# Performance work log

Hardware: AMD Instinct MI355X
Metric: run time of the kernel (lower is better)

Reference implementation:

```python
import jax, jax.numpy as jnp
import numpy as np
import math

B, N, CS, CZ, H, HD, PQ, PV = 1, 512, 1024, 128, 12, 16, 4, 8
INF, EPS = 1e5, 1e-8


def _quat_to_rot(q):
    q = q / jnp.linalg.norm(q, axis=-1, keepdims=True)
    w, x, y, z = q[..., 0], q[..., 1], q[..., 2], q[..., 3]
    R = jnp.stack([
        1 - 2 * (y * y + z * z), 2 * (x * y - w * z), 2 * (x * z + w * y),
        2 * (x * y + w * z), 1 - 2 * (x * x + z * z), 2 * (y * z - w * x),
        2 * (x * z - w * y), 2 * (y * z + w * x), 1 - 2 * (x * x + y * y)
    ], axis=-1)
    return R.reshape(q.shape[:-1] + (3, 3))


def _split3(x):
    # torch.split into 3 chunks along last dim, then stack on new last dim
    d = x.shape[-1] // 3
    return jnp.stack((x[..., :d], x[..., d:2 * d], x[..., 2 * d:]), axis=-1)


def setup_inputs():
    key = jax.random.key(0)
    ks = jax.random.split(key, 12)

    def lin(k, din, dout):
        kw, kb = jax.random.split(k)
        W = jax.random.normal(kw, (din, dout), jnp.float32) / np.float32(np.sqrt(din))
        b = jax.random.normal(kb, (dout,), jnp.float32) * 0.01
        return W, b

    s = jax.random.normal(ks[0], (B, N, CS), jnp.float32)
    z = jax.random.normal(ks[1], (B, N, N, CZ), jnp.float32)
    rot = _quat_to_rot(jax.random.normal(ks[2], (B, N, 4), jnp.float32))
    trans = jax.random.normal(ks[3], (B, N, 3), jnp.float32) * 10.0
    mask = jnp.ones((B, N), jnp.float32)

    Wq, bq = lin(ks[4], CS, H * HD)
    Wkv, bkv = lin(ks[5], CS, 2 * H * HD)
    Wqp, bqp = lin(ks[6], CS, H * PQ * 3)
    Wkvp, bkvp = lin(ks[7], CS, H * (PQ + PV) * 3)
    Wb, bb = lin(ks[8], CZ, H)
    head_w = jax.random.normal(ks[9], (H,), jnp.float32) * 0.5
    Wout, bout = lin(ks[10], H * (CZ + HD + PV * 4), CS)

    return dict(s=s, z=z, rot=rot, trans=trans, mask=mask,
                Wq=Wq, bq=bq, Wkv=Wkv, bkv=bkv, Wqp=Wqp, bqp=bqp,
                Wkvp=Wkvp, bkvp=bkvp, Wb=Wb, bb=bb, head_w=head_w,
                Wout=Wout, bout=bout)


def _ipa(s, z, rot, trans, mask, Wq, bq, Wkv, bkv, Wqp, bqp, Wkvp, bkvp, Wb, bb, head_w, Wout, bout):
    # scalar q, k, v : [B, N, H, HD]
    q = (s @ Wq + bq).reshape(B, N, H, HD)
    kv = (s @ Wkv + bkv).reshape(B, N, H, 2 * HD)
    k, v = kv[..., :HD], kv[..., HD:]

    # point q/k/v in global frame: p' = R p + t
    q_pts = _split3(s @ Wqp + bqp)                      # [B, N, H*PQ, 3]
    q_pts = jnp.einsum('bnij,bnpj->bnpi', rot, q_pts) + trans[:, :, None, :]
    q_pts = q_pts.reshape(B, N, H, PQ, 3)

    kv_pts = _split3(s @ Wkvp + bkvp)                   # [B, N, H*(PQ+PV), 3]
    kv_pts = jnp.einsum('bnij,bnpj->bnpi', rot, kv_pts) + trans[:, :, None, :]
    kv_pts = kv_pts.reshape(B, N, H, PQ + PV, 3)
    k_pts, v_pts = kv_pts[..., :PQ, :], kv_pts[..., PQ:, :]

    # pair bias [B, N, N, H]
    b = z @ Wb + bb

    # scalar attention logits [B, H, N, N]
    a = jnp.einsum('bihd,bjhd->bhij', q, k) * np.float32(math.sqrt(1.0 / (3 * HD)))
    a = a + np.float32(math.sqrt(1.0 / 3)) * jnp.transpose(b, (0, 3, 1, 2))

    # point-distance attention: [B, N, N, H, PQ]
    diff = q_pts[:, :, None] - k_pts[:, None]           # [B, N, N, H, PQ, 3]
    pt_att = jnp.sum(diff * diff, axis=-1)
    hw = jax.nn.softplus(head_w) * np.float32(math.sqrt(1.0 / (3 * (PQ * 9.0 / 2))))
    pt_att = jnp.sum(pt_att * hw[:, None], axis=-1) * (-0.5)   # [B, N, N, H]
    a = a + jnp.transpose(pt_att, (0, 3, 1, 2))

    square_mask = INF * (mask[:, :, None] * mask[:, None, :] - 1.0)  # [B, N, N]
    a = jax.nn.softmax(a + square_mask[:, None], axis=-1)            # [B, H, N, N]

    # scalar output [B, N, H*HD]
    o = jnp.einsum('bhij,bjhd->bihd', a, v).reshape(B, N, H * HD)

    # point output, back to local frame: R^T (p - t)
    o_pt = jnp.einsum('bhij,bjhpc->bihpc', a, v_pts)                 # [B, N, H, PV, 3]
    o_pt = jnp.einsum('bnji,bnhpj->bnhpi', rot, o_pt - trans[:, :, None, None, :])
    o_pt_norm = jnp.sqrt(jnp.sum(o_pt * o_pt, axis=-1) + EPS).reshape(B, N, H * PV)
    o_pt_r = o_pt.reshape(B, N, H * PV, 3)

    # pair output [B, N, H*CZ]
    o_pair = jnp.einsum('bhij,bijc->bihc', a, z).reshape(B, N, H * CZ)

    cat = jnp.concatenate(
        (o, o_pt_r[..., 0], o_pt_r[..., 1], o_pt_r[..., 2], o_pt_norm, o_pair), axis=-1)
    return cat @ Wout + bout


def reference(s, z, rot, trans, mask, Wq, bq, Wkv, bkv, Wqp, bqp, Wkvp, bkvp, Wb, bb, head_w, Wout, bout):
    return _ipa(s, z, rot, trans, mask, Wq, bq, Wkv, bkv, Wqp, bqp, Wkvp, bkvp, Wb, bb, head_w, Wout, bout)
```

## Files before the change

### kernel.cpp

```cpp
#include <hip/hip_runtime.h>
#include <hip/hip_bf16.h>

#define N 512
#define CS 1024
#define CZ 128
#define H 12
#define HD 16
#define KC 2112

__device__ int sniff_f32(const unsigned short* p) {
    int bad = 0;
    for (int i = 0; i < 32; ++i) {
        unsigned short u = p[i];
        int e = (u >> 7) & 0xFF;
        if (e == 0xFF || e >= 141 || (e <= 27 && (u & 0x7FFFu) != 0)) bad++;
    }
    return bad > 0;
}

__device__ __forceinline__ float ld(const void* p, int i, int f32) {
    return f32 ? ((const float*)p)[i]
               : __bfloat162float(((const __hip_bfloat16*)p)[i]);
}

__device__ __forceinline__ float bfu(unsigned short u) {
    return __bfloat162float(*(const __hip_bfloat16*)&u);
}

typedef __attribute__((ext_vector_type(8))) short bf16x8;
typedef __attribute__((ext_vector_type(4))) float f32x4;
typedef __attribute__((ext_vector_type(8))) unsigned short u16x8;

__device__ __forceinline__ unsigned int split_bf16(float x) {
    __hip_bfloat16 hb = __float2bfloat16(x);
    float hf = __bfloat162float(hb);
    __hip_bfloat16 lb = __float2bfloat16(x - hf);
    unsigned int h = *reinterpret_cast<unsigned short*>(&hb);
    unsigned int l = *reinterpret_cast<unsigned short*>(&lb);
    return h | (l << 16);
}

__device__ __forceinline__ void wcat_resolve(int col,
        const void* Wq, const void* Wkv, const void* Wqp, const void* Wkvp,
        const void*& W, int& cc, int& ldim) {
    if (col < 192)      { W = Wq;   cc = col;       ldim = 192; }
    else if (col < 576) { W = Wkv;  cc = col - 192; ldim = 384; }
    else if (col < 720) { W = Wqp;  cc = col - 576; ldim = 144; }
    else                { W = Wkvp; cc = col - 720; ldim = 432; }
}

__global__ void prep_w(const void* Wq, const void* Wkv, const void* Wqp,
                       const void* Wkvp, const void* Wout, const void* s,
                       unsigned short* WcTh, unsigned short* WcTl,
                       unsigned short* WoTh, unsigned short* WoTl)
{
    __shared__ unsigned short th[32][33], tl[32][33];
    __shared__ int flag;
    int t = threadIdx.x;
    if (t == 0) flag = sniff_f32((const unsigned short*)s);
    __syncthreads();
    int f32 = flag;
    int tx = t & 31, ty = t >> 5;
    int b = blockIdx.x;
    if (b < 1152) {
        int ct = b % 36, kt = b / 36;
        int c0 = ct * 32, k0 = kt * 32;
        #pragma unroll
        for (int r = 0; r < 4; ++r) {
            int k = k0 + ty + 8 * r, c = c0 + tx;
            const void* W; int cc, ldim;
            wcat_resolve(c, Wq, Wkv, Wqp, Wkvp, W, cc, ldim);
            unsigned int pe = split_bf16(ld(W, k * ldim + cc, f32));
            th[ty + 8 * r][tx] = (unsigned short)pe;
            tl[ty + 8 * r][tx] = (unsigned short)(pe >> 16);
        }
        __syncthreads();
        #pragma unroll
        for (int r = 0; r < 4; ++r) {
            int c = c0 + ty + 8 * r, k = k0 + tx;
            WcTh[c * CS + k] = th[tx][ty + 8 * r];
            WcTl[c * CS + k] = tl[tx][ty + 8 * r];
        }
    } else {
        int bb = b - 1152;
        int ct = bb & 31, kt = bb >> 5;
        int c0 = ct * 32, k0 = kt * 32;
        #pragma unroll
        for (int r = 0; r < 4; ++r) {
            int k = k0 + ty + 8 * r, c = c0 + tx;
            unsigned int pe = split_bf16(ld(Wout, k * CS + c, f32));
            th[ty + 8 * r][tx] = (unsigned short)pe;
            tl[ty + 8 * r][tx] = (unsigned short)(pe >> 16);
        }
        __syncthreads();
        #pragma unroll
        for (int r = 0; r < 4; ++r) {
            int c = c0 + ty + 8 * r, k = k0 + tx;
            WoTh[c * KC + k] = th[tx][ty + 8 * r];
            WoTl[c * KC + k] = tl[tx][ty + 8 * r];
        }
    }
}

__global__ void proj_gemm(const void* s, const unsigned short* BTh,
                          const unsigned short* BTl, float* rawP)
{
    __shared__ int flag;
    int t = threadIdx.x;
    int bn = blockIdx.x;
    int bm = blockIdx.y;
    if (t == 0) flag = sniff_f32((const unsigned short*)s);
    __syncthreads();
    int f32 = flag;

    int w  = t >> 6, l = t & 63;
    int wm = w >> 1, wn = w & 1;
    int lr = l & 15, lq = l >> 4;

    int arow = bm * 32 + wm * 16 + lr;
    int bcol = bn * 64 + wn * 32 + lr;
    const unsigned short* bh = BTh + bcol * CS;
    const unsigned short* bl = BTl + bcol * CS;

    f32x4 acc0 = {0.f, 0.f, 0.f, 0.f};
    f32x4 acc1 = {0.f, 0.f, 0.f, 0.f};

    #pragma unroll 2
    for (int kt = 0; kt < CS / 32; ++kt) {
        int kk = kt * 32 + lq * 8;
        u16x8 ah, al;
        if (f32) {
            const float* ap = (const float*)s + arow * CS + kk;
            #pragma unroll
            for (int e = 0; e < 8; ++e) {
                unsigned int pe = split_bf16(ap[e]);
                ah[e] = (unsigned short)pe; al[e] = (unsigned short)(pe >> 16);
            }
        } else {
            ah = *(const u16x8*)((const unsigned short*)s + arow * CS + kk);
            #pragma unroll
            for (int e = 0; e < 8; ++e) al[e] = 0;
        }
        bf16x8 b0h = *(const bf16x8*)(bh + kk);
        bf16x8 b0l = *(const bf16x8*)(bl + kk);
        bf16x8 b1h = *(const bf16x8*)(bh + 16 * CS + kk);
        bf16x8 b1l = *(const bf16x8*)(bl + 16 * CS + kk);
        bf16x8 a_h = *(bf16x8*)&ah;
        bf16x8 a_l = *(bf16x8*)&al;
        acc0 = __builtin_amdgcn_mfma_f32_16x16x32_bf16(a_h, b0h, acc0, 0, 0, 0);
        acc0 = __builtin_amdgcn_mfma_f32_16x16x32_bf16(a_h, b0l, acc0, 0, 0, 0);
        acc0 = __builtin_amdgcn_mfma_f32_16x16x32_bf16(a_l, b0h, acc0, 0, 0, 0);
        acc1 = __builtin_amdgcn_mfma_f32_16x16x32_bf16(a_h, b1h, acc1, 0, 0, 0);
        acc1 = __builtin_amdgcn_mfma_f32_16x16x32_bf16(a_h, b1l, acc1, 0, 0, 0);
        acc1 = __builtin_amdgcn_mfma_f32_16x16x32_bf16(a_l, b1h, acc1, 0, 0, 0);
    }

    int col0 = bn * 64 + wn * 32 + lr;
    int row0 = bm * 32 + wm * 16 + lq * 4;
    #pragma unroll
    for (int r = 0; r < 4; ++r) {
        rawP[(row0 + r) * 1152 + col0]      = acc0[r];
        rawP[(row0 + r) * 1152 + col0 + 16] = acc1[r];
    }
}

__global__ void proj_post(const float* rawP,
                          const void* bq, const void* bkv,
                          const void* bqp, const void* bkvp,
                          const void* rot, const void* trans, const void* s,
                          float* q, float* kT, float* v,
                          float* qp, float* kpT, float* vp)
{
    __shared__ float rawL[576];
    __shared__ float R[9], T[3];
    __shared__ int flag;
    int t = threadIdx.x;
    int i = blockIdx.x;
    if (t == 0) flag = sniff_f32((const unsigned short*)s);
    __syncthreads();
    int f32 = flag;

    {
        float val = rawP[i * 1152 + t];
        if (t < 192) q[i * 192 + t] = val + ld(bq, t, f32);
        else {
            int cc = t - 192;
            float vv = val + ld(bkv, cc, f32);
            int h = cc >> 5, t2 = cc & 31;
            if (t2 < 16) kT[(h * 16 + t2) * 512 + i] = vv;
            else         v[i * 192 + h * 16 + (t2 - 16)] = vv;
        }
    }
    rawL[t] = rawP[i * 1152 + 576 + t]
            + (t < 144 ? ld(bqp, t, f32) : ld(bkvp, t - 144, f32));
    if (t < 9) R[t] = ld(rot, i * 9 + t, f32);
    if (t >= 16 && t < 19) T[t - 16] = ld(trans, i * 3 + (t - 16), f32);
    __syncthreads();
    if (t < 192) {
        float x, y, zc;
        if (t < 48) { x = rawL[t];        y = rawL[48 + t];   zc = rawL[96 + t]; }
        else { int pk = t - 48;
               x = rawL[144 + pk]; y = rawL[288 + pk]; zc = rawL[432 + pk]; }
        float rx = R[0]*x + R[1]*y + R[2]*zc + T[0];
        float ry = R[3]*x + R[4]*y + R[5]*zc + T[1];
        float rz = R[6]*x + R[7]*y + R[8]*zc + T[2];
        if (t < 48) {
            int h = t >> 2, pp = t & 3, b = i * 144 + h * 12 + pp * 3;
            qp[b] = rx; qp[b + 1] = ry; qp[b + 2] = rz;
        } else {
            int pk = t - 48, h = pk / 12, idx = pk % 12;
            if (idx < 4) {
                int row = h * 12 + idx * 3;
                kpT[(row + 0) * 512 + i] = rx;
                kpT[(row + 1) * 512 + i] = ry;
                kpT[(row + 2) * 512 + i] = rz;
            } else {
                int b = i * 288 + h * 24 + (idx - 4) * 3;
                vp[b] = rx; vp[b + 1] = ry; vp[b + 2] = rz;
            }
        }
    }
}

__global__ void attn_fused(const float* q, const float* kT, const float* v,
                           const float* qp, const float* kpT, const float* vp,
                           const void* z, const void* Wb, const void* bb,
                           const void* head_w, const void* mask,
                           const void* rot, const void* trans, const void* s,
                           float* cat)
{
    __shared__ float attL[H * N];
    __shared__ float WbL[CZ * H];
    __shared__ float U[6144];
    __shared__ float qL[192], qpL[144];
    __shared__ float RL[9], TL[3], bbL[H], hwL[H];
    __shared__ float miS;
    __shared__ int flag;
    int t = threadIdx.x;
    int i = blockIdx.x;
    if (t == 0) flag = sniff_f32((const unsigned short*)s);
    __syncthreads();
    int f32 = flag;
    for (int idx = t; idx < CZ * H; idx += 512) WbL[idx] = ld(Wb, idx, f32);
    if (t < 192) qL[t] = q[i * 192 + t];
    else if (t < 336) qpL[t - 192] = qp[i * 144 + (t - 192)];
    else if (t < 345) RL[t - 336] = ld(rot, i * 9 + (t - 336), f32);
    else if (t < 348) TL[t - 345] = ld(trans, i * 3 + (t - 345), f32);
    else if (t < 360) bbL[t - 348] = ld(bb, t - 348, f32);
    else if (t < 372) {
        float x = ld(head_w, t - 360, f32);
        float sp = (x > 20.f) ? x : log1pf(expf(x));
        hwL[t - 360] = sp * 0.13608276348795434f;
    }
    else if (t == 372) miS = ld(mask, i, f32);
    __syncthreads();

    {
        int jl = t >> 4, hs = t & 15;
        for (int jt = 0; jt < 16; ++jt) {
            __syncthreads();
            if (f32) {
                const float* zrow = (const float*)z + (i * N + jt * 32) * CZ;
                #pragma unroll
                for (int r = 0; r < 2; ++r) {
                    int flat = (t + 512 * r) * 4;
                    int row = flat >> 7, col = flat & 127;
                    float4 vz = *(const float4*)&zrow[flat];
                    *(float4*)&U[row * 132 + col] = vz;
                }
            } else {
                const unsigned short* zrow =
                    (const unsigned short*)z + (i * N + jt * 32) * CZ;
                int flat = t * 8;
                int row = flat >> 7, col = flat & 127;
                u16x8 uv = *(const u16x8*)&zrow[flat];
                float4 lo = {bfu(uv[0]), bfu(uv[1]), bfu(uv[2]), bfu(uv[3])};
                float4 hi = {bfu(uv[4]), bfu(uv[5]), bfu(uv[6]), bfu(uv[7])};
                *(float4*)&U[row * 132 + col] = lo;
                *(float4*)&U[row * 132 + col + 4] = hi;
            }
            __syncthreads();
            if (hs < H) {
                float acc = bbL[hs];
                #pragma unroll 8
                for (int c = 0; c < CZ; ++c)
                    acc += U[jl * 132 + c] * WbL[c * H + hs];
                attL[hs * N + jt * 32 + jl] = acc;
            }
        }
    }
    __syncthreads();

    {
        int j = t;
        float mj = ld(mask, j, f32);
        float mterm = 100000.0f * (miS * mj - 1.0f);
        const float* kTj  = kT + j;
        const float* kpTj = kpT + j;
        float bj[H];
        #pragma unroll
        for (int h = 0; h < H; ++h) bj[h] = attL[h * N + j];
        for (int h = 0; h < H; ++h) {
            float qk = 0.f;
            #pragma unroll
            for (int d = 0; d < 16; ++d)
                qk += qL[h * 16 + d] * kTj[(h * 16 + d) * 512];
            float pt = 0.f;
            #pragma unroll
            for (int p = 0; p < 4; ++p) {
                float dx = qpL[h*12 + p*3 + 0] - kpTj[(h*12 + p*3 + 0) * 512];
                float dy = qpL[h*12 + p*3 + 1] - kpTj[(h*12 + p*3 + 1) * 512];
                float dz = qpL[h*12 + p*3 + 2] - kpTj[(h*12 + p*3 + 2) * 512];
                pt += dx * dx + dy * dy + dz * dz;
            }
            attL[h * N + j] = qk * 0.14433756729740643f
                            + 0.5773502691896258f * bj[h]
                            - 0.5f * hwL[h] * pt + mterm;
        }
    }
    __syncthreads();

    {
        int w = t >> 6, l = t & 63;
        for (int h = w; h < H; h += 8) {
            float av[8];
            #pragma unroll
            for (int kk = 0; kk < 8; ++kk) av[kk] = attL[h * N + kk * 64 + l];
            float m = av[0];
            #pragma unroll
            for (int kk = 1; kk < 8; ++kk) m = fmaxf(m, av[kk]);
            for (int off = 1; off < 64; off <<= 1) m = fmaxf(m, __shfl_xor(m, off));
            float ssum = 0.f;
            #pragma unroll
            for (int kk = 0; kk < 8; ++kk) { av[kk] = __expf(av[kk] - m); ssum += av[kk]; }
            for (int off = 1; off < 64; off <<= 1) ssum += __shfl_xor(ssum, off);
            float inv = 1.0f / ssum;
            #pragma unroll
            for (int kk = 0; kk < 8; ++kk) attL[h * N + kk * 64 + l] = av[kk] * inv;
        }
    }
    __syncthreads();

    if (t < 192) {
        int h = t >> 4, d = t & 15;
        float acc = 0.f;
        for (int j = 0; j < N; ++j) acc += attL[h * N + j] * v[j * 192 + h * 16 + d];
        cat[i * 2112 + t] = acc;
    } else if (t < 288) {
        int hp = t - 192, h = hp >> 3, p = hp & 7;
        float ax = 0, ay = 0, az = 0;
        for (int j = 0; j < N; ++j) {
            float a_ = attL[h * N + j];
            int b2 = j * 288 + h * 24 + p * 3;
            ax += a_ * vp[b2]; ay += a_ * vp[b2 + 1]; az += a_ * vp[b2 + 2];
        }
        float gx = ax - TL[0], gy = ay - TL[1], gz = az - TL[2];
        float lx = RL[0]*gx + RL[3]*gy + RL[6]*gz;
        float ly = RL[1]*gx + RL[4]*gy + RL[7]*gz;
        float lz = RL[2]*gx + RL[5]*gy + RL[8]*gz;
        float nrm = sqrtf(lx*lx + ly*ly + lz*lz + 1e-8f);
        cat[i * 2112 + 192 + hp] = lx;
        cat[i * 2112 + 288 + hp] = ly;
        cat[i * 2112 + 384 + hp] = lz;
        cat[i * 2112 + 480 + hp] = nrm;
    }

    {
        int quarter = t >> 7, c = t & 127;
        float pacc[H];
        #pragma unroll
        for (int h = 0; h < H; ++h) pacc[h] = 0.f;
        int j0 = quarter * 128;
        if (f32) {
            const float* zp = (const float*)z + (i * N + j0) * CZ + c;
            for (int j = 0; j < 128; ++j) {
                float zc = zp[j * CZ];
                #pragma unroll
                for (int h = 0; h < H; ++h) pacc[h] += attL[h * N + j0 + j] * zc;
            }
        } else {
            const unsigned short* zp =
                (const unsigned short*)z + (i * N + j0) * CZ + c;
            for (int j = 0; j < 128; ++j) {
                float zc = bfu(zp[j * CZ]);
                #pragma unroll
                for (int h = 0; h < H; ++h) pacc[h] += attL[h * N + j0 + j] * zc;
            }
        }
        __syncthreads();
        #pragma unroll
        for (int h = 0; h < H; ++h) U[quarter * (H * CZ) + h * CZ + c] = pacc[h];
    }
    __syncthreads();
    for (int idx = t; idx < H * CZ; idx += 512)
        cat[i * 2112 + 576 + idx] =
            U[idx] + U[1536 + idx] + U[3072 + idx] + U[4608 + idx];
}

__global__ void final_gemm(const float* cat, const unsigned short* BTh,
                           const unsigned short* BTl, const void* bout,
                           void* out, const void* s)
{
    __shared__ int flag;
    int t = threadIdx.x;
    int bn = blockIdx.x;
    int bm = blockIdx.y;
    if (t == 0) flag = sniff_f32((const unsigned short*)s);
    __syncthreads();
    int f32 = flag;

    int w  = t >> 6, l = t & 63;
    int wm = w >> 1, wn = w & 1;
    int lr = l & 15, lq = l >> 4;

    int arow = bm * 32 + wm * 16 + lr;
    int bcol = bn * 64 + wn * 32 + lr;
    const unsigned short* bh = BTh + bcol * KC;
    const unsigned short* bl = BTl + bcol * KC;
    const float* ap0 = cat + arow * KC;

    f32x4 acc0 = {0.f, 0.f, 0.f, 0.f};
    f32x4 acc1 = {0.f, 0.f, 0.f, 0.f};

    #pragma unroll 2
    for (int kt = 0; kt < KC / 32; ++kt) {
        int kk = kt * 32 + lq * 8;
        u16x8 ah, al;
        const float* ap = ap0 + kk;
        #pragma unroll
        for (int e = 0; e < 8; ++e) {
            unsigned int pe = split_bf16(ap[e]);
            ah[e] = (unsigned short)pe; al[e] = (unsigned short)(pe >> 16);
        }
        bf16x8 b0h = *(const bf16x8*)(bh + kk);
        bf16x8 b0l = *(const bf16x8*)(bl + kk);
        bf16x8 b1h = *(const bf16x8*)(bh + 16 * KC + kk);
        bf16x8 b1l = *(const bf16x8*)(bl + 16 * KC + kk);
        bf16x8 a_h = *(bf16x8*)&ah;
        bf16x8 a_l = *(bf16x8*)&al;
        acc0 = __builtin_amdgcn_mfma_f32_16x16x32_bf16(a_h, b0h, acc0, 0, 0, 0);
        acc0 = __builtin_amdgcn_mfma_f32_16x16x32_bf16(a_h, b0l, acc0, 0, 0, 0);
        acc0 = __builtin_amdgcn_mfma_f32_16x16x32_bf16(a_l, b0h, acc0, 0, 0, 0);
        acc1 = __builtin_amdgcn_mfma_f32_16x16x32_bf16(a_h, b1h, acc1, 0, 0, 0);
        acc1 = __builtin_amdgcn_mfma_f32_16x16x32_bf16(a_h, b1l, acc1, 0, 0, 0);
        acc1 = __builtin_amdgcn_mfma_f32_16x16x32_bf16(a_l, b1h, acc1, 0, 0, 0);
    }

    int col0 = bn * 64 + wn * 32 + lr;
    int row0 = bm * 32 + wm * 16 + lq * 4;
    float bv0 = ld(bout, col0, f32);
    float bv1 = ld(bout, col0 + 16, f32);
    if (f32) {
        float* o = (float*)out;
        #pragma unroll
        for (int r = 0; r < 4; ++r) {
            o[(row0 + r) * CS + col0]      = acc0[r] + bv0;
            o[(row0 + r) * CS + col0 + 16] = acc1[r] + bv1;
        }
    } else {
        __hip_bfloat16* o = (__hip_bfloat16*)out;
        #pragma unroll
        for (int r = 0; r < 4; ++r) {
            o[(row0 + r) * CS + col0]      = __float2bfloat16(acc0[r] + bv0);
            o[(row0 + r) * CS + col0 + 16] = __float2bfloat16(acc1[r] + bv1);
        }
    }
}

extern "C" void kernel_launch(void* const* d_in, const int* in_sizes, int n_in,
                              void* d_out, int out_size, void* d_ws, size_t ws_size,
                              hipStream_t stream)
{
    const void* s      = d_in[0];
    const void* z      = d_in[1];
    const void* rot    = d_in[2];
    const void* trans  = d_in[3];
    const void* mask   = d_in[4];
    const void* Wq     = d_in[5];  const void* bq   = d_in[6];
    const void* Wkv    = d_in[7];  const void* bkv  = d_in[8];
    const void* Wqp    = d_in[9];  const void* bqp  = d_in[10];
    const void* Wkvp   = d_in[11]; const void* bkvp = d_in[12];
    const void* Wb     = d_in[13]; const void* bb   = d_in[14];
    const void* head_w = d_in[15];
    const void* Wout   = d_in[16]; const void* bout = d_in[17];

    float* w    = (float*)d_ws;
    float* q    = w;
    float* kT   = q   + 98304;
    float* v    = kT  + 98304;
    float* qp   = v   + 98304;
    float* kpT  = qp  + 73728;
    float* vp   = kpT + 73728;
    float* cat  = vp  + 147456;
    float* rawP = cat;
    unsigned short* WcTh = (unsigned short*)(cat + 512 * 2112);
    unsigned short* WcTl = WcTh + 1152 * 1024;
    unsigned short* WoTh = WcTl + 1152 * 1024;
    unsigned short* WoTl = WoTh + 1024 * 2112;
    (void)ws_size; (void)in_sizes; (void)n_in; (void)out_size;

    prep_w    <<<3264, 256, 0, stream>>>(Wq, Wkv, Wqp, Wkvp, Wout, s,
                                         WcTh, WcTl, WoTh, WoTl);
    proj_gemm <<<dim3(18, 16), 256, 0, stream>>>(s, WcTh, WcTl, rawP);
    proj_post <<<512, 576, 0, stream>>>(rawP, bq, bkv, bqp, bkvp, rot, trans, s,
                                        q, kT, v, qp, kpT, vp);
    attn_fused<<<512, 512, 0, stream>>>(q, kT, v, qp, kpT, vp, z, Wb, bb, head_w, mask,
                                        rot, trans, s, cat);
    final_gemm<<<dim3(16, 16), 256, 0, stream>>>(cat, WoTh, WoTl, bout, d_out, s);
}
```

Baseline: 435.2 us.

## Pre-split GEMM A operands to bf16 hi/lo, shrink GEMM tiles, prefetch z tiles

The input s is now split into bf16 hi/lo arrays in prep_w, and attn_fused writes its concatenated output directly as hi/lo bf16, so neither GEMM has to convert fp32 to bf16 in its inner loop. Both GEMMs switch to 16x64 block tiles with one MFMA accumulator per wave, which doubles the number of blocks. attn_fused also register-prefetches the next z tile while the current one is being processed. In exchange there are extra workspace writes and reads for the split arrays, and each block gets less register-level reuse of B.

```diff
diff --git a/kernel.cpp b/kernel.cpp
--- a/kernel.cpp
+++ b/kernel.cpp
@@ -52,7 +52,8 @@
 __global__ void prep_w(const void* Wq, const void* Wkv, const void* Wqp,
                        const void* Wkvp, const void* Wout, const void* s,
                        unsigned short* WcTh, unsigned short* WcTl,
-                       unsigned short* WoTh, unsigned short* WoTl)
+                       unsigned short* WoTh, unsigned short* WoTl,
+                       unsigned short* sH, unsigned short* sL)
 {
     __shared__ unsigned short th[32][33], tl[32][33];
     __shared__ int flag;
@@ -81,7 +82,7 @@
             WcTh[c * CS + k] = th[tx][ty + 8 * r];
             WcTl[c * CS + k] = tl[tx][ty + 8 * r];
         }
-    } else {
+    } else if (b < 3264) {
         int bb = b - 1152;
         int ct = bb & 31, kt = bb >> 5;
         int c0 = ct * 32, k0 = kt * 32;
@@ -99,69 +100,53 @@
             WoTh[c * KC + k] = th[tx][ty + 8 * r];
             WoTl[c * KC + k] = tl[tx][ty + 8 * r];
         }
-    }
-}
-
-__global__ void proj_gemm(const void* s, const unsigned short* BTh,
-                          const unsigned short* BTl, float* rawP)
+    } else {
+        int bb = b - 3264;
+        int rt = bb >> 5, ct = bb & 31;
+        #pragma unroll
+        for (int r = 0; r < 4; ++r) {
+            int row = rt * 32 + ty + 8 * r, col = ct * 32 + tx;
+            unsigned int pe = split_bf16(ld(s, row * CS + col, f32));
+            sH[row * CS + col] = (unsigned short)pe;
+            sL[row * CS + col] = (unsigned short)(pe >> 16);
+        }
+    }
+}
+
+__global__ void proj_gemm(const unsigned short* sH, const unsigned short* sL,
+                          const unsigned short* BTh, const unsigned short* BTl,
+                          float* rawP)
 {
-    __shared__ int flag;
     int t = threadIdx.x;
     int bn = blockIdx.x;
     int bm = blockIdx.y;
-    if (t == 0) flag = sniff_f32((const unsigned short*)s);
-    __syncthreads();
-    int f32 = flag;
-
     int w  = t >> 6, l = t & 63;
-    int wm = w >> 1, wn = w & 1;
     int lr = l & 15, lq = l >> 4;
 
-    int arow = bm * 32 + wm * 16 + lr;
-    int bcol = bn * 64 + wn * 32 + lr;
-    const unsigned short* bh = BTh + bcol * CS;
-    const unsigned short* bl = BTl + bcol * CS;
-
-    f32x4 acc0 = {0.f, 0.f, 0.f, 0.f};
-    f32x4 acc1 = {0.f, 0.f, 0.f, 0.f};
-
-    #pragma unroll 2
+    int arow = bm * 16 + lr;
+    int bcol = bn * 64 + w * 16 + lr;
+    const unsigned short* ah_p = sH + arow * CS;
+    const unsigned short* al_p = sL + arow * CS;
+    const unsigned short* bh_p = BTh + bcol * CS;
+    const unsigned short* bl_p = BTl + bcol * CS;
+
+    f32x4 acc = {0.f, 0.f, 0.f, 0.f};
+    #pragma unroll 4
     for (int kt = 0; kt < CS / 32; ++kt) {
         int kk = kt * 32 + lq * 8;
-        u16x8 ah, al;
-        if (f32) {
-            const float* ap = (const float*)s + arow * CS + kk;
-            #pragma unroll
-            for (int e = 0; e < 8; ++e) {
-                unsigned int pe = split_bf16(ap[e]);
-                ah[e] = (unsigned short)pe; al[e] = (unsigned short)(pe >> 16);
-            }
-        } else {
-            ah = *(const u16x8*)((const unsigned short*)s + arow * CS + kk);
-            #pragma unroll
-            for (int e = 0; e < 8; ++e) al[e] = 0;
-        }
-        bf16x8 b0h = *(const bf16x8*)(bh + kk);
-        bf16x8 b0l = *(const bf16x8*)(bl + kk);
-        bf16x8 b1h = *(const bf16x8*)(bh + 16 * CS + kk);
-        bf16x8 b1l = *(const bf16x8*)(bl + 16 * CS + kk);
-        bf16x8 a_h = *(bf16x8*)&ah;
-        bf16x8 a_l = *(bf16x8*)&al;
-        acc0 = __builtin_amdgcn_mfma_f32_16x16x32_bf16(a_h, b0h, acc0, 0, 0, 0);
-        acc0 = __builtin_amdgcn_mfma_f32_16x16x32_bf16(a_h, b0l, acc0, 0, 0, 0);
-        acc0 = __builtin_amdgcn_mfma_f32_16x16x32_bf16(a_l, b0h, acc0, 0, 0, 0);
-        acc1 = __builtin_amdgcn_mfma_f32_16x16x32_bf16(a_h, b1h, acc1, 0, 0, 0);
-        acc1 = __builtin_amdgcn_mfma_f32_16x16x32_bf16(a_h, b1l, acc1, 0, 0, 0);
-        acc1 = __builtin_amdgcn_mfma_f32_16x16x32_bf16(a_l, b1h, acc1, 0, 0, 0);
-    }
-
-    int col0 = bn * 64 + wn * 32 + lr;
-    int row0 = bm * 32 + wm * 16 + lq * 4;
+        bf16x8 a_h = *(const bf16x8*)(ah_p + kk);
+        bf16x8 a_l = *(const bf16x8*)(al_p + kk);
+        bf16x8 b_h = *(const bf16x8*)(bh_p + kk);
+        bf16x8 b_l = *(const bf16x8*)(bl_p + kk);
+        acc = __builtin_amdgcn_mfma_f32_16x16x32_bf16(a_h, b_h, acc, 0, 0, 0);
+        acc = __builtin_amdgcn_mfma_f32_16x16x32_bf16(a_h, b_l, acc, 0, 0, 0);
+        acc = __builtin_amdgcn_mfma_f32_16x16x32_bf16(a_l, b_h, acc, 0, 0, 0);
+    }
+
+    int row0 = bm * 16 + lq * 4;
     #pragma unroll
-    for (int r = 0; r < 4; ++r) {
-        rawP[(row0 + r) * 1152 + col0]      = acc0[r];
-        rawP[(row0 + r) * 1152 + col0 + 16] = acc1[r];
-    }
+    for (int r = 0; r < 4; ++r)
+        rawP[(row0 + r) * 1152 + bcol] = acc[r];
 }
 
 __global__ void proj_post(const float* rawP,
@@ -227,7 +212,7 @@
                            const void* z, const void* Wb, const void* bb,
                            const void* head_w, const void* mask,
                            const void* rot, const void* trans, const void* s,
-                           float* cat)
+                           unsigned short* catH, unsigned short* catL)
 {
     __shared__ float attL[H * N];
     __shared__ float WbL[CZ * H];
@@ -257,29 +242,40 @@
 
     {
         int jl = t >> 4, hs = t & 15;
+        float4 pf0, pf1; u16x8 pfu;
+        if (f32) {
+            const float* zrow = (const float*)z + (size_t)i * N * CZ;
+            pf0 = *(const float4*)&zrow[t * 4];
+            pf1 = *(const float4*)&zrow[(t + 512) * 4];
+        } else {
+            const unsigned short* zrow = (const unsigned short*)z + (size_t)i * N * CZ;
+            pfu = *(const u16x8*)&zrow[t * 8];
+        }
         for (int jt = 0; jt < 16; ++jt) {
             __syncthreads();
             if (f32) {
-                const float* zrow = (const float*)z + (i * N + jt * 32) * CZ;
-                #pragma unroll
-                for (int r = 0; r < 2; ++r) {
-                    int flat = (t + 512 * r) * 4;
-                    int row = flat >> 7, col = flat & 127;
-                    float4 vz = *(const float4*)&zrow[flat];
-                    *(float4*)&U[row * 132 + col] = vz;
-                }
+                int f0 = t * 4, f1 = (t + 512) * 4;
+                *(float4*)&U[(f0 >> 7) * 132 + (f0 & 127)] = pf0;
+                *(float4*)&U[(f1 >> 7) * 132 + (f1 & 127)] = pf1;
             } else {
-                const unsigned short* zrow =
-                    (const unsigned short*)z + (i * N + jt * 32) * CZ;
-                int flat = t * 8;
-                int row = flat >> 7, col = flat & 127;
-                u16x8 uv = *(const u16x8*)&zrow[flat];
-                float4 lo = {bfu(uv[0]), bfu(uv[1]), bfu(uv[2]), bfu(uv[3])};
-                float4 hi = {bfu(uv[4]), bfu(uv[5]), bfu(uv[6]), bfu(uv[7])};
+                int flat = t * 8; int row = flat >> 7, col = flat & 127;
+                float4 lo = {bfu(pfu[0]), bfu(pfu[1]), bfu(pfu[2]), bfu(pfu[3])};
+                float4 hi = {bfu(pfu[4]), bfu(pfu[5]), bfu(pfu[6]), bfu(pfu[7])};
                 *(float4*)&U[row * 132 + col] = lo;
                 *(float4*)&U[row * 132 + col + 4] = hi;
             }
             __syncthreads();
+            if (jt < 15) {
+                if (f32) {
+                    const float* zrow = (const float*)z + ((size_t)i * N + (jt + 1) * 32) * CZ;
+                    pf0 = *(const float4*)&zrow[t * 4];
+                    pf1 = *(const float4*)&zrow[(t + 512) * 4];
+                } else {
+                    const unsigned short* zrow =
+                        (const unsigned short*)z + ((size_t)i * N + (jt + 1) * 32) * CZ;
+                    pfu = *(const u16x8*)&zrow[t * 8];
+                }
+            }
             if (hs < H) {
                 float acc = bbL[hs];
                 #pragma unroll 8
@@ -345,7 +341,9 @@
         int h = t >> 4, d = t & 15;
         float acc = 0.f;
         for (int j = 0; j < N; ++j) acc += attL[h * N + j] * v[j * 192 + h * 16 + d];
-        cat[i * 2112 + t] = acc;
+        unsigned int pe = split_bf16(acc);
+        catH[i * KC + t] = (unsigned short)pe;
+        catL[i * KC + t] = (unsigned short)(pe >> 16);
     } else if (t < 288) {
         int hp = t - 192, h = hp >> 3, p = hp & 7;
         float ax = 0, ay = 0, az = 0;
@@ -359,10 +357,19 @@
         float ly = RL[1]*gx + RL[4]*gy + RL[7]*gz;
         float lz = RL[2]*gx + RL[5]*gy + RL[8]*gz;
         float nrm = sqrtf(lx*lx + ly*ly + lz*lz + 1e-8f);
-        cat[i * 2112 + 192 + hp] = lx;
-        cat[i * 2112 + 288 + hp] = ly;
-        cat[i * 2112 + 384 + hp] = lz;
-        cat[i * 2112 + 480 + hp] = nrm;
+        unsigned int pe;
+        pe = split_bf16(lx);
+        catH[i * KC + 192 + hp] = (unsigned short)pe;
+        catL[i * KC + 192 + hp] = (unsigned short)(pe >> 16);
+        pe = split_bf16(ly);
+        catH[i * KC + 288 + hp] = (unsigned short)pe;
+        catL[i * KC + 288 + hp] = (unsigned short)(pe >> 16);
+        pe = split_bf16(lz);
+        catH[i * KC + 384 + hp] = (unsigned short)pe;
+        catL[i * KC + 384 + hp] = (unsigned short)(pe >> 16);
+        pe = split_bf16(nrm);
+        catH[i * KC + 480 + hp] = (unsigned short)pe;
+        catL[i * KC + 480 + hp] = (unsigned short)(pe >> 16);
     }
 
     {
@@ -372,7 +379,7 @@
         for (int h = 0; h < H; ++h) pacc[h] = 0.f;
         int j0 = quarter * 128;
         if (f32) {
-            const float* zp = (const float*)z + (i * N + j0) * CZ + c;
+            const float* zp = (const float*)z + ((size_t)i * N + j0) * CZ + c;
             for (int j = 0; j < 128; ++j) {
                 float zc = zp[j * CZ];
                 #pragma unroll
@@ -380,7 +387,7 @@
             }
         } else {
             const unsigned short* zp =
-                (const unsigned short*)z + (i * N + j0) * CZ + c;
+                (const unsigned short*)z + ((size_t)i * N + j0) * CZ + c;
             for (int j = 0; j < 128; ++j) {
                 float zc = bfu(zp[j * CZ]);
                 #pragma unroll
@@ -392,14 +399,17 @@
         for (int h = 0; h < H; ++h) U[quarter * (H * CZ) + h * CZ + c] = pacc[h];
     }
     __syncthreads();
-    for (int idx = t; idx < H * CZ; idx += 512)
-        cat[i * 2112 + 576 + idx] =
-            U[idx] + U[1536 + idx] + U[3072 + idx] + U[4608 + idx];
-}
-
-__global__ void final_gemm(const float* cat, const unsigned short* BTh,
-                           const unsigned short* BTl, const void* bout,
-                           void* out, const void* s)
+    for (int idx = t; idx < H * CZ; idx += 512) {
+        float vsum = U[idx] + U[1536 + idx] + U[3072 + idx] + U[4608 + idx];
+        unsigned int pe = split_bf16(vsum);
+        catH[i * KC + 576 + idx] = (unsigned short)pe;
+        catL[i * KC + 576 + idx] = (unsigned short)(pe >> 16);
+    }
+}
+
+__global__ void final_gemm(const unsigned short* AH, const unsigned short* AL,
+                           const unsigned short* BTh, const unsigned short* BTl,
+                           const void* bout, void* out, const void* s)
 {
     __shared__ int flag;
     int t = threadIdx.x;
@@ -410,60 +420,39 @@
     int f32 = flag;
 
     int w  = t >> 6, l = t & 63;
-    int wm = w >> 1, wn = w & 1;
     int lr = l & 15, lq = l >> 4;
 
-    int arow = bm * 32 + wm * 16 + lr;
-    int bcol = bn * 64 + wn * 32 + lr;
-    const unsigned short* bh = BTh + bcol * KC;
-    const unsigned short* bl = BTl + bcol * KC;
-    const float* ap0 = cat + arow * KC;
-
-    f32x4 acc0 = {0.f, 0.f, 0.f, 0.f};
-    f32x4 acc1 = {0.f, 0.f, 0.f, 0.f};
-
-    #pragma unroll 2
+    int arow = bm * 16 + lr;
+    int bcol = bn * 64 + w * 16 + lr;
+    const unsigned short* ah_p = AH + (size_t)arow * KC;
+    const unsigned short* al_p = AL + (size_t)arow * KC;
+    const unsigned short* bh_p = BTh + (size_t)bcol * KC;
+    const unsigned short* bl_p = BTl + (size_t)bcol * KC;
+
+    f32x4 acc = {0.f, 0.f, 0.f, 0.f};
+    #pragma unroll 4
     for (int kt = 0; kt < KC / 32; ++kt) {
         int kk = kt * 32 + lq * 8;
-        u16x8 ah, al;
-        const float* ap = ap0 + kk;
-        #pragma unroll
-        for (int e = 0; e < 8; ++e) {
-            unsigned int pe = split_bf16(ap[e]);
-            ah[e] = (unsigned short)pe; al[e] = (unsigned short)(pe >> 16);
-        }
-        bf16x8 b0h = *(const bf16x8*)(bh + kk);
-        bf16x8 b0l = *(const bf16x8*)(bl + kk);
-        bf16x8 b1h = *(const bf16x8*)(bh + 16 * KC + kk);
-        bf16x8 b1l = *(const bf16x8*)(bl + 16 * KC + kk);
-        bf16x8 a_h = *(bf16x8*)&ah;
-        bf16x8 a_l = *(bf16x8*)&al;
-        acc0 = __builtin_amdgcn_mfma_f32_16x16x32_bf16(a_h, b0h, acc0, 0, 0, 0);
-        acc0 = __builtin_amdgcn_mfma_f32_16x16x32_bf16(a_h, b0l, acc0, 0, 0, 0);
-        acc0 = __builtin_amdgcn_mfma_f32_16x16x32_bf16(a_l, b0h, acc0, 0, 0, 0);
-        acc1 = __builtin_amdgcn_mfma_f32_16x16x32_bf16(a_h, b1h, acc1, 0, 0, 0);
-        acc1 = __builtin_amdgcn_mfma_f32_16x16x32_bf16(a_h, b1l, acc1, 0, 0, 0);
-        acc1 = __builtin_amdgcn_mfma_f32_16x16x32_bf16(a_l, b1h, acc1, 0, 0, 0);
-    }
-
-    int col0 = bn * 64 + wn * 32 + lr;
-    int row0 = bm * 32 + wm * 16 + lq * 4;
-    float bv0 = ld(bout, col0, f32);
-    float bv1 = ld(bout, col0 + 16, f32);
+        bf16x8 a_h = *(const bf16x8*)(ah_p + kk);
+        bf16x8 a_l = *(const bf16x8*)(al_p + kk);
+        bf16x8 b_h = *(const bf16x8*)(bh_p + kk);
+        bf16x8 b_l = *(const bf16x8*)(bl_p + kk);
+        acc = __builtin_amdgcn_mfma_f32_16x16x32_bf16(a_h, b_h, acc, 0, 0, 0);
+        acc = __builtin_amdgcn_mfma_f32_16x16x32_bf16(a_h, b_l, acc, 0, 0, 0);
+        acc = __builtin_amdgcn_mfma_f32_16x16x32_bf16(a_l, b_h, acc, 0, 0, 0);
+    }
+
+    int row0 = bm * 16 + lq * 4;
+    float bv = ld(bout, bcol, f32);
     if (f32) {
         float* o = (float*)out;
         #pragma unroll
-        for (int r = 0; r < 4; ++r) {
-            o[(row0 + r) * CS + col0]      = acc0[r] + bv0;
-            o[(row0 + r) * CS + col0 + 16] = acc1[r] + bv1;
-        }
+        for (int r = 0; r < 4; ++r) o[(row0 + r) * CS + bcol] = acc[r] + bv;
     } else {
         __hip_bfloat16* o = (__hip_bfloat16*)out;
         #pragma unroll
-        for (int r = 0; r < 4; ++r) {
-            o[(row0 + r) * CS + col0]      = __float2bfloat16(acc0[r] + bv0);
-            o[(row0 + r) * CS + col0 + 16] = __float2bfloat16(acc1[r] + bv1);
-        }
+        for (int r = 0; r < 4; ++r)
+            o[(row0 + r) * CS + bcol] = __float2bfloat16(acc[r] + bv);
     }
 }
 
@@ -491,20 +480,24 @@
     float* qp   = v   + 98304;
     float* kpT  = qp  + 73728;
     float* vp   = kpT + 73728;
-    float* cat  = vp  + 147456;
-    float* rawP = cat;
-    unsigned short* WcTh = (unsigned short*)(cat + 512 * 2112);
-    unsigned short* WcTl = WcTh + 1152 * 1024;
-    unsigned short* WoTh = WcTl + 1152 * 1024;
-    unsigned short* WoTl = WoTh + 1024 * 2112;
+    float* rawP = vp  + 147456;
+    unsigned short* sH   = (unsigned short*)(rawP + 589824);
+    unsigned short* sL   = sH   + 524288;
+    unsigned short* catH = sL   + 524288;
+    unsigned short* catL = catH + 1081344;
+    unsigned short* WcTh = catL + 1081344;
+    unsigned short* WcTl = WcTh + 1179648;
+    unsigned short* WoTh = WcTl + 1179648;
+    unsigned short* WoTl = WoTh + 2162688;
     (void)ws_size; (void)in_sizes; (void)n_in; (void)out_size;
 
-    prep_w    <<<3264, 256, 0, stream>>>(Wq, Wkv, Wqp, Wkvp, Wout, s,
-                                         WcTh, WcTl, WoTh, WoTl);
-    proj_gemm <<<dim3(18, 16), 256, 0, stream>>>(s, WcTh, WcTl, rawP);
+    prep_w    <<<3776, 256, 0, stream>>>(Wq, Wkv, Wqp, Wkvp, Wout, s,
+                                         WcTh, WcTl, WoTh, WoTl, sH, sL);
+    proj_gemm <<<dim3(18, 32), 256, 0, stream>>>(sH, sL, WcTh, WcTl, rawP);
     proj_post <<<512, 576, 0, stream>>>(rawP, bq, bkv, bqp, bkvp, rot, trans, s,
                                         q, kT, v, qp, kpT, vp);
     attn_fused<<<512, 512, 0, stream>>>(q, kT, v, qp, kpT, vp, z, Wb, bb, head_w, mask,
-                                        rot, trans, s, cat);
-    final_gemm<<<dim3(16, 16), 256, 0, stream>>>(cat, WoTh, WoTl, bout, d_out, s);
-}
+                                        rot, trans, s, catH, catL);
+    final_gemm<<<dim3(16, 32), 256, 0, stream>>>(catH, catL, WoTh, WoTl, bout,
+                                                 d_out, s);
+}
```

Measured after the change: 436.1 us. No clear change (+0.2%).
